# Optimization experiments

Measured on AMD Instinct MI355X. Metric: run time of the kernel, lower is better.

The kernel has to match this reference:

```python
import jax, jax.numpy as jnp
import numpy as np

HEADS = 16
D_MODEL = 1024
D_K = D_MODEL // HEADS
B, S = 2, 2048
NEG = -1000000000.0


def setup_inputs() -> dict:
    key = jax.random.key(0)
    ks = jax.random.split(key, 8)
    q = jax.random.normal(ks[0], (B, S, D_MODEL), dtype=jnp.float32)
    k = jax.random.normal(ks[1], (B, S, D_MODEL), dtype=jnp.float32)
    v = jax.random.normal(ks[2], (B, S, D_MODEL), dtype=jnp.float32)
    mask = jax.random.randint(ks[3], (B, 1, S, S), 0, 2) > 0  # True = masked
    scale = 1.0 / np.sqrt(D_MODEL)
    Wq = jax.random.normal(ks[4], (D_MODEL, D_MODEL), dtype=jnp.float32) * scale
    Wk = jax.random.normal(ks[5], (D_MODEL, D_MODEL), dtype=jnp.float32) * scale
    Wv = jax.random.normal(ks[6], (D_MODEL, D_MODEL), dtype=jnp.float32) * scale
    Wo = jax.random.normal(ks[7], (D_MODEL, D_MODEL), dtype=jnp.float32) * scale
    return {"q": q, "k": k, "v": v, "mask": mask,
            "Wq": Wq, "Wk": Wk, "Wv": Wv, "Wo": Wo}


def reference(q, k, v, mask, Wq, Wk, Wv, Wo):
    b, s, _ = q.shape
    # torch Linear: x @ W.T ; reshape to [B, H, S, d_k]
    def proj(x, W):
        return (x @ W.T).reshape(b, -1, HEADS, D_K).transpose(0, 2, 1, 3)
    qh, kh, vh = proj(q, Wq), proj(k, Wk), proj(v, Wv)
    # scaled dot-product attention; scale uses d_k (key.shape[-1] after reshape)
    att = jnp.einsum('bhqd,bhkd->bhqk', qh, kh) / jnp.sqrt(jnp.float32(D_K))
    att = jnp.where(mask, NEG, att)
    att = jax.nn.softmax(att, axis=-1)
    out = jnp.einsum('bhqk,bhkd->bhqd', att, vh)  # [B,H,S,d_k]
    out = out.transpose(0, 2, 1, 3).reshape(b, -1, D_MODEL)
    return out @ Wo.T  # dropout is identity at inference
```

## Files before the change

kernel.cpp:

```cpp
#include <hip/hip_runtime.h>

typedef unsigned short u16;
typedef unsigned int   u32;
typedef unsigned char  u8;
typedef unsigned long long u64;
typedef __attribute__((ext_vector_type(8))) short bf16x8;
typedef __attribute__((ext_vector_type(4))) float f32x4;
typedef __attribute__((ext_vector_type(16))) float f32x16;

__device__ __forceinline__ u16 f2b(float f) {
  union { float f; u32 u; } v; v.f = f;
  u32 u = v.u;
  return (u16)((u + 0x7fffu + ((u >> 16) & 1u)) >> 16);
}
__device__ __forceinline__ u32 pk2(u16 lo, u16 hi) { return (u32)lo | ((u32)hi << 16); }

__device__ __forceinline__ float fexp2(float x) { return __builtin_amdgcn_exp2f(x); }

__device__ __forceinline__ u32 cvtpk(float lo, float hi) {
  u32 r;
  asm("v_cvt_pk_bf16_f32 %0, %1, %2" : "=v"(r) : "v"(lo), "v"(hi));
  return r;
}

__device__ __forceinline__ void swap32(u32& a, u32& b) {
  asm("v_permlane32_swap_b32 %0, %1" : "+v"(a), "+v"(b));
}

__device__ __forceinline__ void glds16(const u16* g, u16* l) {
  __builtin_amdgcn_global_load_lds((const __attribute__((address_space(1))) void*)g,
                                   (__attribute__((address_space(3))) void*)l, 16, 0, 0);
}

__global__ __launch_bounds__(256) void mask_detect(const u8* __restrict__ raw,
                                                   int* __restrict__ flag) {
  __shared__ int c1s, c2s;
  if (threadIdx.x == 0) { c1s = 0; c2s = 0; }
  __syncthreads();
  const uint4* p = (const uint4*)raw;
  u32 a1 = 0, a2 = 0;
  for (int i = threadIdx.x; i < 8192; i += 256) {
    uint4 x = p[i];
    u32 o = x.x | x.y | x.z | x.w;
    a1 |= o & 0x0000ff00u;
    a2 |= o & 0xffff0000u;
  }
  if (a1) atomicOr(&c1s, 1);
  if (a2) atomicOr(&c2s, 1);
  __syncthreads();
  if (threadIdx.x == 0) *flag = c1s ? 2 : (c2s ? 1 : 0);
}

__global__ __launch_bounds__(256) void mask_bits(const u8* __restrict__ raw,
                                                 u64* __restrict__ out,
                                                 const int* __restrict__ flag) {
  int f = *flag;
  int i = blockIdx.x * 256 + threadIdx.x;
  bool bit;
  if (f == 2)      bit = raw[i] != 0;
  else if (f == 0) bit = ((const int*)raw)[i] != 0;
  else             bit = ((const float*)raw)[i] != 0.0f;
  u64 b = __ballot(bit);
  if ((threadIdx.x & 63) == 0) out[i >> 6] = b;
}

__global__ __launch_bounds__(256) void conv_all(
    const float* __restrict__ W0, const float* __restrict__ W1,
    const float* __restrict__ W2, const float* __restrict__ W3,
    const float* __restrict__ A0, const float* __restrict__ A1,
    const float* __restrict__ A2,
    u16* __restrict__ o0, u16* __restrict__ o1, u16* __restrict__ o2,
    u16* __restrict__ o3, u16* __restrict__ o4, u16* __restrict__ o5,
    u16* __restrict__ o6) {
  int gid = blockIdx.x * 256 + threadIdx.x;
  const float* src; u16* dst; int off;
  if (gid < 524288) {
    int wz = gid >> 17; off = (gid & 131071) * 8;
    src = wz == 0 ? W0 : wz == 1 ? W1 : wz == 2 ? W2 : W3;
    dst = wz == 0 ? o0 : wz == 1 ? o1 : wz == 2 ? o2 : o3;
  } else {
    int g2 = gid - 524288;
    int az = g2 >> 19; off = (g2 & 524287) * 8;
    src = az == 0 ? A0 : az == 1 ? A1 : A2;
    dst = az == 0 ? o4 : az == 1 ? o5 : o6;
  }
  float4 a = *(const float4*)(src + off), b2 = *(const float4*)(src + off + 4);
  uint4 t;
  t.x = pk2(f2b(a.x), f2b(a.y));   t.y = pk2(f2b(a.z), f2b(a.w));
  t.z = pk2(f2b(b2.x), f2b(b2.y)); t.w = pk2(f2b(b2.z), f2b(b2.w));
  *(uint4*)(dst + off) = t;
}

template<int CF32>
__device__ __forceinline__ void gemm_body(
    const u16* __restrict__ Av, const u16* __restrict__ Bv, void* __restrict__ Cv,
    int N, int K, int m0, int n0, float cscale, u16* As, u16* Bs) {
  const int tid = threadIdx.x;
  const int lane = tid & 63, w = tid >> 6;
  const int lr = lane & 15, lg = lane >> 4;
  const int wm = (w >> 1) * 64, wn = (w & 1) * 64;
  const int srow = lane >> 3;
  const int selem = (((lane & 7) ^ srow) << 3);
  const int rsw = (lr & 7) << 3;

  f32x4 acc[4][4];
#pragma unroll
  for (int mi = 0; mi < 4; ++mi)
#pragma unroll
    for (int ni = 0; ni < 4; ++ni)
      acc[mi][ni] = (f32x4){0.f, 0.f, 0.f, 0.f};

#define GSTAGE(buf, k0_)                                                       \
  do {                                                                         \
    _Pragma("unroll")                                                          \
    for (int r_ = 0; r_ < 4; ++r_) {                                           \
      const int c_ = w * 4 + r_;                                               \
      const int row_ = c_ * 8 + srow;                                          \
      glds16(Av + (size_t)(m0 + row_) * K + (k0_) + selem, As + (buf) * 8192 + c_ * 512); \
      glds16(Bv + (size_t)(n0 + row_) * K + (k0_) + selem, Bs + (buf) * 8192 + c_ * 512); \
    }                                                                          \
  } while (0)

  GSTAGE(0, 0);
  __syncthreads();
  int cur = 0;
  for (int k0 = 0; k0 < K; k0 += 64) {
    if (k0 + 64 < K) GSTAGE(cur ^ 1, k0 + 64);
    bf16x8 af[4][2], bfv[4][2];
#pragma unroll
    for (int mi = 0; mi < 4; ++mi)
#pragma unroll
      for (int kk = 0; kk < 2; ++kk)
        af[mi][kk] = *(bf16x8*)&As[cur * 8192 + (wm + mi * 16 + lr) * 64 + ((kk * 32 + lg * 8) ^ rsw)];
#pragma unroll
    for (int ni = 0; ni < 4; ++ni)
#pragma unroll
      for (int kk = 0; kk < 2; ++kk)
        bfv[ni][kk] = *(bf16x8*)&Bs[cur * 8192 + (wn + ni * 16 + lr) * 64 + ((kk * 32 + lg * 8) ^ rsw)];
    __builtin_amdgcn_s_setprio(1);
#pragma unroll
    for (int mi = 0; mi < 4; ++mi)
#pragma unroll
      for (int ni = 0; ni < 4; ++ni)
#pragma unroll
        for (int kk = 0; kk < 2; ++kk)
          acc[mi][ni] = __builtin_amdgcn_mfma_f32_16x16x32_bf16(
              af[mi][kk], bfv[ni][kk], acc[mi][ni], 0, 0, 0);
    __builtin_amdgcn_s_setprio(0);
    __syncthreads();
    cur ^= 1;
  }
#undef GSTAGE
#pragma unroll
  for (int mi = 0; mi < 4; ++mi)
#pragma unroll
    for (int ni = 0; ni < 4; ++ni)
#pragma unroll
      for (int r = 0; r < 4; ++r) {
        int m = m0 + wm + mi * 16 + lg * 4 + r;
        int n = n0 + wn + ni * 16 + lr;
        float vv = acc[mi][ni][r] * cscale;
        if (CF32) ((float*)Cv)[(size_t)m * N + n] = vv;
        else      ((u16*)Cv)[(size_t)m * N + n] = f2b(vv);
      }
}

__global__ __launch_bounds__(256) void gemm_qkv(
    const u16* __restrict__ qb, const u16* __restrict__ kb, const u16* __restrict__ vb,
    const u16* __restrict__ Wqb, const u16* __restrict__ Wkb, const u16* __restrict__ Wvb,
    u16* __restrict__ Qb, u16* __restrict__ Kb, u16* __restrict__ VTb, float qscale) {
  __shared__ __align__(16) u16 As[2 * 8192];
  __shared__ __align__(16) u16 Bs[2 * 8192];
  const int z = blockIdx.z;
  const u16 *Av, *Bv; u16* Cv; int N, bxx, by; float cs = 1.0f;
  if (z < 2) {
    Av = z ? kb : qb; Bv = z ? Wkb : Wqb; Cv = z ? Kb : Qb;
    N = 1024; bxx = blockIdx.x & 7; by = blockIdx.x >> 3;
    if (!z) cs = qscale;
  } else {
    Av = Wvb; Bv = vb; Cv = VTb;
    N = 4096; bxx = blockIdx.x & 31; by = blockIdx.x >> 5;
  }
  gemm_body<0>(Av, Bv, Cv, N, 1024, by * 128, bxx * 128, cs, As, Bs);
}

__global__ __launch_bounds__(256) void gemm_o(
    const u16* __restrict__ Ob, const u16* __restrict__ Wob, float* __restrict__ C) {
  __shared__ __align__(16) u16 As[2 * 8192];
  __shared__ __align__(16) u16 Bs[2 * 8192];
  gemm_body<1>(Ob, Wob, C, 1024, 1024, blockIdx.y * 128, blockIdx.x * 128, 1.0f, As, Bs);
}

__global__ __launch_bounds__(256) void flash5(const u16* __restrict__ Q,
                                              const u16* __restrict__ K,
                                              const u16* __restrict__ VT,
                                              const u64* __restrict__ mpk,
                                              u16* __restrict__ O) {
  __shared__ __align__(16) u16 Ks[2][4096];
  __shared__ __align__(16) u16 Vs[2][4096];
  __shared__ float rs[4][32];
  const int tid = threadIdx.x, lane = tid & 63, w = tid >> 6;
  const int c = lane & 31, h = lane >> 5;
  const int q0 = blockIdx.x * 128, head = blockIdx.y, b = blockIdx.z;
  const int qw = q0 + w * 32;
  const size_t kbase = (size_t)b * 2048 * 1024 + (size_t)head * 64;
  const size_t vbase = (size_t)head * 64 * 4096 + (size_t)b * 2048;
  const int srow = lane >> 3;
  const int selem = (((lane & 7) ^ srow) << 3);
  const int rswc = (c & 7) << 3;

  bf16x8 qf[4];
#pragma unroll
  for (int kd = 0; kd < 4; ++kd)
    qf[kd] = *(const bf16x8*)&Q[kbase + (size_t)(qw + c) * 1024 + 16 * kd + 8 * h];

  f32x16 accO0, accO1;
#pragma unroll
  for (int i = 0; i < 16; ++i) { accO0[i] = 0.f; accO1[i] = 0.f; }
  float lsum = 0.f;

  const u64* mrp = mpk + ((size_t)b * 2048 + qw + c) * 32;

#define STAGE(buf, t)                                                          \
  do {                                                                         \
    const int k0_ = (t) * 64;                                                  \
    _Pragma("unroll")                                                          \
    for (int r_ = 0; r_ < 2; ++r_) {                                           \
      const int c_ = w * 2 + r_;                                               \
      const int row_ = c_ * 8 + srow;                                          \
      glds16(K + kbase + (size_t)(k0_ + row_) * 1024 + selem, &Ks[buf][c_ * 512]); \
    }                                                                          \
    _Pragma("unroll")                                                          \
    for (int r_ = 0; r_ < 2; ++r_) {                                           \
      const int c_ = w * 2 + r_;                                               \
      const int row_ = c_ * 8 + srow;                                          \
      glds16(VT + vbase + (size_t)row_ * 4096 + k0_ + selem, &Vs[buf][c_ * 512]); \
    }                                                                          \
  } while (0)

  STAGE(0, 0);
  u64 mb_next = mrp[0];
  __syncthreads();

  int cur = 0;
  for (int kt = 0; kt < 32; ++kt) {
    const u64 mb = mb_next;
    if (kt + 1 < 32) {
      STAGE(cur ^ 1, kt + 1);
      mb_next = mrp[kt + 1];
    }
    const u16* ks = Ks[cur];
    const u16* vs = Vs[cur];
    f32x16 s0, s1;
#pragma unroll
    for (int i = 0; i < 16; ++i) { s0[i] = 0.f; s1[i] = 0.f; }
    __builtin_amdgcn_s_setprio(1);
#pragma unroll
    for (int kd = 0; kd < 4; ++kd) {
      bf16x8 kf0 = *(bf16x8*)&ks[c * 64 + ((16 * kd + 8 * h) ^ rswc)];
      s0 = __builtin_amdgcn_mfma_f32_32x32x16_bf16(kf0, qf[kd], s0, 0, 0, 0);
      bf16x8 kf1 = *(bf16x8*)&ks[(32 + c) * 64 + ((16 * kd + 8 * h) ^ rswc)];
      s1 = __builtin_amdgcn_mfma_f32_32x32x16_bf16(kf1, qf[kd], s1, 0, 0, 0);
    }
    __builtin_amdgcn_s_setprio(0);
    u32 pw[2][4][2];
#pragma unroll
    for (int kb = 0; kb < 2; ++kb) {
      const u32 m32 = (u32)(mb >> (32 * kb + 4 * h));
      float pp[16];
#pragma unroll
      for (int g = 0; g < 4; ++g)
#pragma unroll
        for (int r = 0; r < 4; ++r) {
          float e = fexp2(kb == 0 ? s0[4 * g + r] : s1[4 * g + r]);
          float pv = ((m32 >> (8 * g + r)) & 1) ? 0.0f : e;
          pp[4 * g + r] = pv;
          lsum += pv;
        }
#pragma unroll
      for (int g = 0; g < 4; ++g)
#pragma unroll
        for (int hh = 0; hh < 2; ++hh)
          pw[kb][g][hh] = cvtpk(pp[4 * g + 2 * hh], pp[4 * g + 2 * hh + 1]);
    }
    __builtin_amdgcn_s_setprio(1);
#pragma unroll
    for (int kb = 0; kb < 2; ++kb)
#pragma unroll
      for (int s = 0; s < 2; ++s) {
        u32 w0 = pw[kb][2 * s][0], w2 = pw[kb][2 * s + 1][0];
        swap32(w0, w2);
        u32 w1 = pw[kb][2 * s][1], w3 = pw[kb][2 * s + 1][1];
        swap32(w1, w3);
        union { u32 u[4]; bf16x8 v; } af;
        af.u[0] = w0; af.u[1] = w1; af.u[2] = w2; af.u[3] = w3;
        const int ksg = kb * 2 + s;
        bf16x8 vf0 = *(bf16x8*)&vs[c * 64 + ((16 * ksg + 8 * h) ^ rswc)];
        accO0 = __builtin_amdgcn_mfma_f32_32x32x16_bf16(af.v, vf0, accO0, 0, 0, 0);
        bf16x8 vf1 = *(bf16x8*)&vs[(32 + c) * 64 + ((16 * ksg + 8 * h) ^ rswc)];
        accO1 = __builtin_amdgcn_mfma_f32_32x32x16_bf16(af.v, vf1, accO1, 0, 0, 0);
      }
    __builtin_amdgcn_s_setprio(0);
    if (kt + 1 < 32) __syncthreads();
    cur ^= 1;
  }
#undef STAGE
  lsum += __shfl_xor(lsum, 32);
  rs[w][c] = lsum;
  const size_t obase = (size_t)b * 2048 * 1024 + (size_t)head * 64;
#pragma unroll
  for (int g = 0; g < 4; ++g)
#pragma unroll
    for (int r = 0; r < 4; ++r) {
      const int qrow = r + 8 * g + 4 * h;
      const float inv = 1.0f / rs[w][qrow];
      const size_t base = obase + (size_t)(qw + qrow) * 1024 + c;
      O[base]      = f2b(accO0[4 * g + r] * inv);
      O[base + 32] = f2b(accO1[4 * g + r] * inv);
    }
}

extern "C" void kernel_launch(void* const* d_in, const int* in_sizes, int n_in,
                              void* d_out, int out_size, void* d_ws, size_t ws_size,
                              hipStream_t stream) {
  const float* q    = (const float*)d_in[0];
  const float* k    = (const float*)d_in[1];
  const float* v    = (const float*)d_in[2];
  const u8*    mask = (const u8*)d_in[3];
  const float* Wq   = (const float*)d_in[4];
  const float* Wk   = (const float*)d_in[5];
  const float* Wv   = (const float*)d_in[6];
  const float* Wo   = (const float*)d_in[7];

  u8* ws = (u8*)d_ws;
  int* flag = (int*)ws;
  u64* mpk  = (u64*)(ws + 256);
  u16* Wqb  = (u16*)(ws + 256 + (1u << 20));
  u16* Wkb  = Wqb + (1 << 20);
  u16* Wvb  = Wkb + (1 << 20);
  u16* Wob  = Wvb + (1 << 20);
  const size_t NE = (size_t)4096 * 1024;
  u16* vb   = Wob + (1 << 20);
  u16* Ob   = vb;
  u16* Qb   = vb + NE;
  u16* Kb   = Qb + NE;
  u16* VTb  = Kb + NE;
  u16* qb   = (u16*)d_out;
  u16* kb   = qb + NE;

  const float LOG2E = 1.4426950408889634f;

  mask_detect<<<1, 256, 0, stream>>>(mask, flag);
  mask_bits<<<32768, 256, 0, stream>>>(mask, mpk, flag);
  conv_all<<<8192, 256, 0, stream>>>(Wq, Wk, Wv, Wo, q, k, v,
                                     Wqb, Wkb, Wvb, Wob, qb, kb, vb);

  gemm_qkv<<<dim3(256, 1, 3), 256, 0, stream>>>(
      qb, kb, vb, Wqb, Wkb, Wvb, Qb, Kb, VTb, 0.125f * LOG2E);

  flash5<<<dim3(16, 16, 2), 256, 0, stream>>>(Qb, Kb, VTb, mpk, Ob);

  gemm_o<<<dim3(8, 32), 256, 0, stream>>>(Ob, Wob, (float*)d_out);
}
```

Baseline: 165.7 us.

## Triple-buffer flash attention K/V tiles and remap blocks for XCD locality

Flash attention now keeps three LDS buffers for K and V and prefetches two tiles ahead. An explicit vmcnt wait plus a single barrier per iteration replaces the old sync-after-compute double buffering. The grid is flattened to 1D, and each block is remapped so that all query blocks of a given (batch, head) pair land on the same XCD, which should improve L2 reuse of K/V. The cost is more LDS per block, which may lower occupancy, and a hand-counted vmcnt value that is fragile if the compiler reorders loads.

```diff
diff --git a/kernel.cpp b/kernel.cpp
--- a/kernel.cpp
+++ b/kernel.cpp
@@ -30,6 +30,11 @@
 __device__ __forceinline__ void glds16(const u16* g, u16* l) {
   __builtin_amdgcn_global_load_lds((const __attribute__((address_space(1))) void*)g,
                                    (__attribute__((address_space(3))) void*)l, 16, 0, 0);
+}
+
+__device__ __forceinline__ void fence() {
+  asm volatile("" ::: "memory");
+  __builtin_amdgcn_sched_barrier(0);
 }
 
 __global__ __launch_bounds__(256) void mask_detect(const u8* __restrict__ raw,
@@ -191,17 +196,22 @@
   gemm_body<1>(Ob, Wob, C, 1024, 1024, blockIdx.y * 128, blockIdx.x * 128, 1.0f, As, Bs);
 }
 
-__global__ __launch_bounds__(256) void flash5(const u16* __restrict__ Q,
+__global__ __launch_bounds__(256) void flash6(const u16* __restrict__ Q,
                                               const u16* __restrict__ K,
                                               const u16* __restrict__ VT,
                                               const u64* __restrict__ mpk,
                                               u16* __restrict__ O) {
-  __shared__ __align__(16) u16 Ks[2][4096];
-  __shared__ __align__(16) u16 Vs[2][4096];
+  __shared__ __align__(16) u16 Ks[3][4096];
+  __shared__ __align__(16) u16 Vs[3][4096];
   __shared__ float rs[4][32];
   const int tid = threadIdx.x, lane = tid & 63, w = tid >> 6;
   const int c = lane & 31, h = lane >> 5;
-  const int q0 = blockIdx.x * 128, head = blockIdx.y, b = blockIdx.z;
+  const int bid = blockIdx.x;
+  const int xcd = bid & 7, j = bid >> 3;
+  const int pair = xcd * 4 + (j >> 4);
+  const int qblk = j & 15;
+  const int head = pair & 15, b = pair >> 4;
+  const int q0 = qblk * 128;
   const int qw = q0 + w * 32;
   const size_t kbase = (size_t)b * 2048 * 1024 + (size_t)head * 64;
   const size_t vbase = (size_t)head * 64 * 4096 + (size_t)b * 2048;
@@ -221,36 +231,40 @@
 
   const u64* mrp = mpk + ((size_t)b * 2048 + qw + c) * 32;
 
-#define STAGE(buf, t)                                                          \
+#define STAGE(kd_, vd_, t)                                                     \
   do {                                                                         \
     const int k0_ = (t) * 64;                                                  \
     _Pragma("unroll")                                                          \
     for (int r_ = 0; r_ < 2; ++r_) {                                           \
       const int c_ = w * 2 + r_;                                               \
       const int row_ = c_ * 8 + srow;                                          \
-      glds16(K + kbase + (size_t)(k0_ + row_) * 1024 + selem, &Ks[buf][c_ * 512]); \
+      glds16(K + kbase + (size_t)(k0_ + row_) * 1024 + selem, (kd_) + c_ * 512); \
     }                                                                          \
     _Pragma("unroll")                                                          \
     for (int r_ = 0; r_ < 2; ++r_) {                                           \
       const int c_ = w * 2 + r_;                                               \
       const int row_ = c_ * 8 + srow;                                          \
-      glds16(VT + vbase + (size_t)row_ * 4096 + k0_ + selem, &Vs[buf][c_ * 512]); \
+      glds16(VT + vbase + (size_t)row_ * 4096 + k0_ + selem, (vd_) + c_ * 512); \
     }                                                                          \
   } while (0)
 
-  STAGE(0, 0);
-  u64 mb_next = mrp[0];
-  __syncthreads();
-
-  int cur = 0;
+  u16 *kA = Ks[0], *kB = Ks[1], *kC = Ks[2];
+  u16 *vA = Vs[0], *vB = Vs[1], *vC = Vs[2];
+  u64 mbA, mbB, mbC = 0;
+  STAGE(kA, vA, 0); fence(); mbA = mrp[0]; fence();
+  STAGE(kB, vB, 1); fence(); mbB = mrp[1]; fence();
+
   for (int kt = 0; kt < 32; ++kt) {
-    const u64 mb = mb_next;
-    if (kt + 1 < 32) {
-      STAGE(cur ^ 1, kt + 1);
-      mb_next = mrp[kt + 1];
+    if (kt < 31) asm volatile("s_waitcnt vmcnt(9)" ::: "memory");
+    else         asm volatile("s_waitcnt vmcnt(0)" ::: "memory");
+    __builtin_amdgcn_s_barrier();
+    __builtin_amdgcn_sched_barrier(0);
+    if (kt + 2 < 32) {
+      STAGE(kC, vC, kt + 2); fence(); mbC = mrp[kt + 2]; fence();
     }
-    const u16* ks = Ks[cur];
-    const u16* vs = Vs[cur];
+    const u16* ks = kA;
+    const u16* vs = vA;
+    const u64 mb = mbA;
     f32x16 s0, s1;
 #pragma unroll
     for (int i = 0; i < 16; ++i) { s0[i] = 0.f; s1[i] = 0.f; }
@@ -301,8 +315,9 @@
         accO1 = __builtin_amdgcn_mfma_f32_32x32x16_bf16(af.v, vf1, accO1, 0, 0, 0);
       }
     __builtin_amdgcn_s_setprio(0);
-    if (kt + 1 < 32) __syncthreads();
-    cur ^= 1;
+    u16* tk = kA; kA = kB; kB = kC; kC = tk;
+    u16* tv = vA; vA = vB; vB = vC; vC = tv;
+    mbA = mbB; mbB = mbC;
   }
 #undef STAGE
   lsum += __shfl_xor(lsum, 32);
@@ -358,7 +373,7 @@
   gemm_qkv<<<dim3(256, 1, 3), 256, 0, stream>>>(
       qb, kb, vb, Wqb, Wkb, Wvb, Qb, Kb, VTb, 0.125f * LOG2E);
 
-  flash5<<<dim3(16, 16, 2), 256, 0, stream>>>(Qb, Kb, VTb, mpk, Ob);
+  flash6<<<512, 256, 0, stream>>>(Qb, Kb, VTb, mpk, Ob);
 
   gemm_o<<<dim3(8, 32), 256, 0, stream>>>(Ob, Wob, (float*)d_out);
 }
```

Measured after the change: 164.6 us. About the same (-0.6%).

## Split attention over two key halves with combine kernel and XCD-aware block mapping

Applied to the files above, without the earlier changes.

The flash attention kernel now splits each query block's 32 key tiles into two halves processed by separate blocks. That doubles the grid to 1024 blocks and maps blocks so each XCD works on the same head and batch groups. Row sums come from an extra MFMA against a ones vector rather than scalar adds. Partial outputs and sums are written to scratch and merged by a new combine kernel. Mask detection is also parallelised across 32 blocks using atomics after a memset. This is meant to raise occupancy and L2 locality, at the cost of extra bf16 partial traffic, a rounding step on the partials, and an additional launch.

```diff
diff --git a/kernel.cpp b/kernel.cpp
--- a/kernel.cpp
+++ b/kernel.cpp
@@ -13,6 +13,9 @@
   u32 u = v.u;
   return (u16)((u + 0x7fffu + ((u >> 16) & 1u)) >> 16);
 }
+__device__ __forceinline__ float b2f(u16 x) {
+  union { u32 u; float f; } v; v.u = ((u32)x) << 16; return v.f;
+}
 __device__ __forceinline__ u32 pk2(u16 lo, u16 hi) { return (u32)lo | ((u32)hi << 16); }
 
 __device__ __forceinline__ float fexp2(float x) { return __builtin_amdgcn_exp2f(x); }
@@ -34,27 +37,23 @@
 
 __global__ __launch_bounds__(256) void mask_detect(const u8* __restrict__ raw,
                                                    int* __restrict__ flag) {
-  __shared__ int c1s, c2s;
-  if (threadIdx.x == 0) { c1s = 0; c2s = 0; }
-  __syncthreads();
-  const uint4* p = (const uint4*)raw;
-  u32 a1 = 0, a2 = 0;
-  for (int i = threadIdx.x; i < 8192; i += 256) {
-    uint4 x = p[i];
-    u32 o = x.x | x.y | x.z | x.w;
-    a1 |= o & 0x0000ff00u;
-    a2 |= o & 0xffff0000u;
-  }
-  if (a1) atomicOr(&c1s, 1);
-  if (a2) atomicOr(&c2s, 1);
-  __syncthreads();
-  if (threadIdx.x == 0) *flag = c1s ? 2 : (c2s ? 1 : 0);
+  int i = blockIdx.x * 256 + threadIdx.x;
+  uint4 x = ((const uint4*)raw)[i];
+  u32 o = x.x | x.y | x.z | x.w;
+  u32 a1 = o & 0x0000ff00u;
+  u32 a2 = o & 0xffff0000u;
+  u64 b1 = __ballot(a1 != 0);
+  u64 b2 = __ballot(a2 != 0);
+  if ((threadIdx.x & 63) == 0) {
+    if (b1) atomicOr(&flag[0], 1);
+    if (b2) atomicOr(&flag[1], 1);
+  }
 }
 
 __global__ __launch_bounds__(256) void mask_bits(const u8* __restrict__ raw,
                                                  u64* __restrict__ out,
                                                  const int* __restrict__ flag) {
-  int f = *flag;
+  int f = flag[0] ? 2 : (flag[1] ? 1 : 0);
   int i = blockIdx.x * 256 + threadIdx.x;
   bool bit;
   if (f == 2)      bit = raw[i] != 0;
@@ -191,18 +190,24 @@
   gemm_body<1>(Ob, Wob, C, 1024, 1024, blockIdx.y * 128, blockIdx.x * 128, 1.0f, As, Bs);
 }
 
-__global__ __launch_bounds__(256) void flash5(const u16* __restrict__ Q,
-                                              const u16* __restrict__ K,
-                                              const u16* __restrict__ VT,
-                                              const u64* __restrict__ mpk,
-                                              u16* __restrict__ O) {
+__global__ __launch_bounds__(256, 4) void flash7(const u16* __restrict__ Q,
+                                                 const u16* __restrict__ K,
+                                                 const u16* __restrict__ VT,
+                                                 const u64* __restrict__ mpk,
+                                                 u16* __restrict__ O0,
+                                                 u16* __restrict__ O1,
+                                                 float* __restrict__ Lp) {
   __shared__ __align__(16) u16 Ks[2][4096];
   __shared__ __align__(16) u16 Vs[2][4096];
-  __shared__ float rs[4][32];
   const int tid = threadIdx.x, lane = tid & 63, w = tid >> 6;
   const int c = lane & 31, h = lane >> 5;
-  const int q0 = blockIdx.x * 128, head = blockIdx.y, b = blockIdx.z;
-  const int qw = q0 + w * 32;
+  const int bid = blockIdx.x;
+  const int xcd = bid & 7, idx = bid >> 3;
+  const int gl = idx >> 4, qblk = idx & 15;
+  const int group = xcd * 8 + gl;
+  const int half = group & 1, head = (group >> 1) & 15, b = group >> 5;
+  const int qw = qblk * 128 + w * 32;
+  const int kt0 = half * 16;
   const size_t kbase = (size_t)b * 2048 * 1024 + (size_t)head * 64;
   const size_t vbase = (size_t)head * 64 * 4096 + (size_t)b * 2048;
   const int srow = lane >> 3;
@@ -214,10 +219,13 @@
   for (int kd = 0; kd < 4; ++kd)
     qf[kd] = *(const bf16x8*)&Q[kbase + (size_t)(qw + c) * 1024 + 16 * kd + 8 * h];
 
-  f32x16 accO0, accO1;
-#pragma unroll
-  for (int i = 0; i < 16; ++i) { accO0[i] = 0.f; accO1[i] = 0.f; }
-  float lsum = 0.f;
+  union { u32 u[4]; bf16x8 v; } ones;
+#pragma unroll
+  for (int i = 0; i < 4; ++i) ones.u[i] = 0x3f803f80u;
+
+  f32x16 accO0, accO1, accL;
+#pragma unroll
+  for (int i = 0; i < 16; ++i) { accO0[i] = 0.f; accO1[i] = 0.f; accL[i] = 0.f; }
 
   const u64* mrp = mpk + ((size_t)b * 2048 + qw + c) * 32;
 
@@ -238,16 +246,16 @@
     }                                                                          \
   } while (0)
 
-  STAGE(0, 0);
-  u64 mb_next = mrp[0];
+  STAGE(0, kt0);
+  u64 mb_next = mrp[kt0];
   __syncthreads();
 
   int cur = 0;
-  for (int kt = 0; kt < 32; ++kt) {
+  for (int t = 0; t < 16; ++t) {
     const u64 mb = mb_next;
-    if (kt + 1 < 32) {
-      STAGE(cur ^ 1, kt + 1);
-      mb_next = mrp[kt + 1];
+    if (t + 1 < 16) {
+      STAGE(cur ^ 1, kt0 + t + 1);
+      mb_next = mrp[kt0 + t + 1];
     }
     const u16* ks = Ks[cur];
     const u16* vs = Vs[cur];
@@ -273,9 +281,7 @@
 #pragma unroll
         for (int r = 0; r < 4; ++r) {
           float e = fexp2(kb == 0 ? s0[4 * g + r] : s1[4 * g + r]);
-          float pv = ((m32 >> (8 * g + r)) & 1) ? 0.0f : e;
-          pp[4 * g + r] = pv;
-          lsum += pv;
+          pp[4 * g + r] = ((m32 >> (8 * g + r)) & 1) ? 0.0f : e;
         }
 #pragma unroll
       for (int g = 0; g < 4; ++g)
@@ -299,25 +305,46 @@
         accO0 = __builtin_amdgcn_mfma_f32_32x32x16_bf16(af.v, vf0, accO0, 0, 0, 0);
         bf16x8 vf1 = *(bf16x8*)&vs[(32 + c) * 64 + ((16 * ksg + 8 * h) ^ rswc)];
         accO1 = __builtin_amdgcn_mfma_f32_32x32x16_bf16(af.v, vf1, accO1, 0, 0, 0);
+        accL  = __builtin_amdgcn_mfma_f32_32x32x16_bf16(af.v, ones.v, accL, 0, 0, 0);
       }
     __builtin_amdgcn_s_setprio(0);
-    if (kt + 1 < 32) __syncthreads();
+    __syncthreads();
     cur ^= 1;
   }
 #undef STAGE
-  lsum += __shfl_xor(lsum, 32);
-  rs[w][c] = lsum;
-  const size_t obase = (size_t)b * 2048 * 1024 + (size_t)head * 64;
+  u16* Op = half ? O1 : O0;
+  const size_t obase = (size_t)b * 2048 + qw;
 #pragma unroll
   for (int g = 0; g < 4; ++g)
 #pragma unroll
     for (int r = 0; r < 4; ++r) {
       const int qrow = r + 8 * g + 4 * h;
-      const float inv = 1.0f / rs[w][qrow];
-      const size_t base = obase + (size_t)(qw + qrow) * 1024 + c;
-      O[base]      = f2b(accO0[4 * g + r] * inv);
-      O[base + 32] = f2b(accO1[4 * g + r] * inv);
+      const size_t row = obase + qrow;
+      const size_t base = row * 1024 + (size_t)head * 64 + c;
+      Op[base]      = f2b(accO0[4 * g + r]);
+      Op[base + 32] = f2b(accO1[4 * g + r]);
+      if (c == 0) Lp[(size_t)half * 65536 + row * 16 + head] = accL[4 * g + r];
     }
+}
+
+__global__ __launch_bounds__(256) void combine(const u16* __restrict__ O0,
+                                               const u16* __restrict__ O1,
+                                               const float* __restrict__ Lp,
+                                               u16* __restrict__ Ob) {
+  int gid = blockIdx.x * 256 + threadIdx.x;
+  int row = gid >> 7, chb = (gid & 127) * 8;
+  int head = chb >> 6;
+  float l0 = Lp[(size_t)row * 16 + head];
+  float l1 = Lp[65536 + (size_t)row * 16 + head];
+  float inv = 1.0f / (l0 + l1);
+  size_t off = (size_t)row * 1024 + chb;
+  union { uint4 q; u16 s[8]; } a, b, o;
+  a.q = *(const uint4*)(O0 + off);
+  b.q = *(const uint4*)(O1 + off);
+#pragma unroll
+  for (int j = 0; j < 8; ++j)
+    o.s[j] = f2b((b2f(a.s[j]) + b2f(b.s[j])) * inv);
+  *(uint4*)(Ob + off) = o.q;
 }
 
 extern "C" void kernel_launch(void* const* d_in, const int* in_sizes, int n_in,
@@ -347,10 +374,14 @@
   u16* VTb  = Kb + NE;
   u16* qb   = (u16*)d_out;
   u16* kb   = qb + NE;
+  u16* Opart0 = qb;
+  u16* Opart1 = kb;
+  float* Lp = (float*)Wqb;
 
   const float LOG2E = 1.4426950408889634f;
 
-  mask_detect<<<1, 256, 0, stream>>>(mask, flag);
+  hipMemsetAsync(flag, 0, 8, stream);
+  mask_detect<<<32, 256, 0, stream>>>(mask, flag);
   mask_bits<<<32768, 256, 0, stream>>>(mask, mpk, flag);
   conv_all<<<8192, 256, 0, stream>>>(Wq, Wk, Wv, Wo, q, k, v,
                                      Wqb, Wkb, Wvb, Wob, qb, kb, vb);
@@ -358,7 +389,8 @@
   gemm_qkv<<<dim3(256, 1, 3), 256, 0, stream>>>(
       qb, kb, vb, Wqb, Wkb, Wvb, Qb, Kb, VTb, 0.125f * LOG2E);
 
-  flash5<<<dim3(16, 16, 2), 256, 0, stream>>>(Qb, Kb, VTb, mpk, Ob);
+  flash7<<<1024, 256, 0, stream>>>(Qb, Kb, VTb, mpk, Opart0, Opart1, Lp);
+  combine<<<2048, 256, 0, stream>>>(Opart0, Opart1, Lp, Ob);
 
   gemm_o<<<dim3(8, 32), 256, 0, stream>>>(Ob, Wob, (float*)d_out);
 }
```

Measured after the change: 161.9 us. 1.02x faster.
